# Performance work log

Hardware: AMD Instinct MI355X
Metric: run time of the kernel (lower is better)

Reference implementation:

```python
import jax, jax.numpy as jnp
import numpy as np

N = 50000
E = 800000
DIM_H = 128
EPS = 1e-5


def _glorot(key, shape):
    fan_in, fan_out = shape[0], shape[1]
    lim = np.sqrt(6.0 / (fan_in + fan_out))
    return jax.random.uniform(key, shape, jnp.float32, -lim, lim)


def setup_inputs() -> dict:
    key = jax.random.key(0)
    ks = jax.random.split(key, 12)
    h = jax.random.normal(ks[0], (N, DIM_H), jnp.float32)
    x = jax.random.normal(ks[1], (N, 3), jnp.float32)
    e = jax.random.randint(ks[2], (2, E), 0, N, jnp.int32)
    dx = jax.random.normal(ks[3], (E, 3), jnp.float32)
    d2 = jax.random.uniform(ks[4], (E, 1), jnp.float32)
    # message_layer.phi params: Linear(2*dim_h+1, dim_h), LayerNorm(dim_h), Linear(dim_h, dim_h)
    W1 = _glorot(ks[5], (2 * DIM_H + 1, DIM_H))
    b1 = jnp.zeros((DIM_H,), jnp.float32)
    g1 = jnp.ones((DIM_H,), jnp.float32)
    beta1 = jnp.zeros((DIM_H,), jnp.float32)
    W2 = _glorot(ks[6], (DIM_H, DIM_H))
    b2 = jnp.zeros((DIM_H,), jnp.float32)
    # outer phi params: Linear(dim_h, dim_h), Linear(dim_h, 1)
    W3 = _glorot(ks[7], (DIM_H, DIM_H))
    b3 = jnp.zeros((DIM_H,), jnp.float32)
    W4 = _glorot(ks[8], (DIM_H, 1))
    b4 = jnp.zeros((1,), jnp.float32)
    return {"h": h, "x": x, "e": e, "dx": dx, "d2": d2,
            "W1": W1, "b1": b1, "g1": g1, "beta1": beta1,
            "W2": W2, "b2": b2, "W3": W3, "b3": b3, "W4": W4, "b4": b4}


def _layernorm(z, g, b):
    mu = jnp.mean(z, axis=-1, keepdims=True)
    var = jnp.mean(jnp.square(z - mu), axis=-1, keepdims=True)
    return (z - mu) * jax.lax.rsqrt(var + EPS) * g + b


def reference(h, x, e, dx, d2, W1, b1, g1, beta1, W2, b2, W3, b3, W4, b4):
    ei, ej = e[0], e[1]
    hi = h[ei]                      # [E, dim_h]
    hj = h[ej]                      # [E, dim_h]
    msg = jnp.concatenate((hi, hj, d2), axis=-1)   # [E, 2*dim_h+1]
    msg = jax.nn.silu(msg @ W1 + b1)
    msg = _layernorm(msg, g1, beta1)
    msg = jax.nn.silu(msg @ W2 + b2)               # [E, dim_h]
    scale = jax.nn.silu(msg @ W3 + b3) @ W4 + b4   # [E, 1]
    vec = dx * scale                               # [E, 3]
    agg = jax.ops.segment_sum(vec, ei, num_segments=N)  # [N, 3]
    return x + agg
```

## Files before the change

kernel.cpp:

```cpp
#include <hip/hip_runtime.h>
#include <hip/hip_bf16.h>
#include <cstdint>

#define NN 50000
#define NE 800000
#define DH 128
#define TILES 50000
#define NCHUNK 4
#define CT (TILES / NCHUNK)

typedef __bf16 bf16;
typedef __bf16 bf16x8 __attribute__((ext_vector_type(8)));
typedef float  f32x4  __attribute__((ext_vector_type(4)));

__device__ __forceinline__ float fast_silu(float x) {
    float e = __expf(-x);
    return x * __builtin_amdgcn_rcpf(1.0f + e);
}

__global__ void prep_kernel(const float* __restrict__ W1, const float* __restrict__ W2,
                            const float* __restrict__ W3, const float* __restrict__ b1,
                            const float* __restrict__ g1, const float* __restrict__ bt1,
                            const float* __restrict__ b2, const float* __restrict__ b3,
                            const float* __restrict__ W4,
                            bf16* __restrict__ w1aT, bf16* __restrict__ w1bT,
                            bf16* __restrict__ w2T,  bf16* __restrict__ w3T,
                            float* __restrict__ smalls) {
    int i = blockIdx.x * 256 + threadIdx.x;
    int n = i >> 7, k = i & 127;
    w1aT[i] = (bf16)W1[k * DH + n];
    w1bT[i] = (bf16)W1[(k + DH) * DH + n];
    w2T[i]  = (bf16)W2[k * DH + n];
    w3T[i]  = (bf16)W3[k * DH + n];
    if (i < DH) {
        smalls[i]          = W1[256 * DH + i];
        smalls[DH + i]     = b1[i];
        smalls[2 * DH + i] = g1[i];
        smalls[3 * DH + i] = bt1[i];
        smalls[4 * DH + i] = b2[i];
        smalls[5 * DH + i] = b3[i];
        smalls[6 * DH + i] = W4[i];
    }
}

__global__ __launch_bounds__(256) void node_kernel(const float* __restrict__ h,
                                                   const bf16* __restrict__ w1aT,
                                                   const bf16* __restrict__ w1bT,
                                                   bf16* __restrict__ An,
                                                   bf16* __restrict__ Bn) {
    int lane = threadIdx.x & 63, wid = threadIdx.x >> 6;
    int r = lane & 15, g = lane >> 4;
    int wt = blockIdx.x * 4 + wid;
    if (wt >= (NN / 16)) return;
    int base = wt * 16;
    int node = base + r;

    bf16x8 ha[4];
#pragma unroll
    for (int s = 0; s < 4; s++) {
        const float* hp = h + (size_t)node * DH + s * 32 + g * 8;
        float4 p0 = *(const float4*)hp;
        float4 p1 = *(const float4*)(hp + 4);
        ha[s][0] = (bf16)p0.x; ha[s][1] = (bf16)p0.y;
        ha[s][2] = (bf16)p0.z; ha[s][3] = (bf16)p0.w;
        ha[s][4] = (bf16)p1.x; ha[s][5] = (bf16)p1.y;
        ha[s][6] = (bf16)p1.z; ha[s][7] = (bf16)p1.w;
    }
#pragma unroll
    for (int t = 0; t < 16; t++) {
        const bf16* wmat = (t < 8) ? w1aT : w1bT;
        int n = (t & 7) * 16 + r;
        f32x4 acc = {0.f, 0.f, 0.f, 0.f};
#pragma unroll
        for (int s = 0; s < 4; s++) {
            bf16x8 wb = *(const bf16x8*)(wmat + n * DH + s * 32 + g * 8);
            acc = __builtin_amdgcn_mfma_f32_16x16x32_bf16(ha[s], wb, acc, 0, 0, 0);
        }
        bf16* dst = (t < 8) ? An : Bn;
#pragma unroll
        for (int jj = 0; jj < 4; jj++)
            dst[(size_t)(base + g * 4 + jj) * DH + (t & 7) * 16 + r] = (bf16)acc[jj];
    }
}

__global__ void init_kernel(const float* __restrict__ x, float* __restrict__ out, int n) {
    int i = blockIdx.x * 256 + threadIdx.x;
    if (i < n) out[i] = x[i];
}

__global__ __launch_bounds__(256) void edgeA_kernel(
    const bf16* __restrict__ An, const bf16* __restrict__ Bn,
    const float* __restrict__ smalls, const int* __restrict__ e,
    const float* __restrict__ d2, bf16* __restrict__ Z, int tile0) {
    __shared__ float sSm[4 * 128];
    int tid = threadIdx.x;
    if (tid < 128) {
#pragma unroll
        for (int a = 0; a < 4; a++) sSm[a * 128 + tid] = smalls[a * 128 + tid];
    }
    __syncthreads();
    const float* s_w1c = sSm;
    const float* s_b1  = sSm + 128;
    const float* s_g1  = sSm + 256;
    const float* s_bt1 = sSm + 384;

    int lane = tid & 63, wid = tid >> 6;
    int r = lane & 15, g = lane >> 4;
    int wgid = blockIdx.x * 4 + wid;
    int nw = gridDim.x * 4;

    for (int lt = wgid; lt < CT; lt += nw) {
        int base = (tile0 + lt) * 16;
        int ei = e[base + r];
        int ej = e[NE + base + r];
        float d2v = d2[base + r];
        const bf16* Ar = An + (size_t)ei * DH;
        const bf16* Br = Bn + (size_t)ej * DH;

        float z[4][8];
#pragma unroll
        for (int s = 0; s < 4; s++) {
            bf16x8 av = *(const bf16x8*)(Ar + s * 32 + g * 8);
            bf16x8 bv = *(const bf16x8*)(Br + s * 32 + g * 8);
#pragma unroll
            for (int j = 0; j < 8; j++) {
                int f = s * 32 + g * 8 + j;
                float zz = (float)av[j] + (float)bv[j] + d2v * s_w1c[f] + s_b1[f];
                z[s][j] = fast_silu(zz);
            }
        }
        float sum = 0.f, sq = 0.f;
#pragma unroll
        for (int s = 0; s < 4; s++)
#pragma unroll
            for (int j = 0; j < 8; j++) { sum += z[s][j]; sq += z[s][j] * z[s][j]; }
        sum += __shfl_xor(sum, 16); sq += __shfl_xor(sq, 16);
        sum += __shfl_xor(sum, 32); sq += __shfl_xor(sq, 32);
        float mu = sum * 0.0078125f;
        float var = sq * 0.0078125f - mu * mu;
        float rs = __builtin_amdgcn_rsqf(var + 1e-5f);

        bf16* zp = Z + (size_t)lt * 2048 + g * 128 + r * 8;
#pragma unroll
        for (int s = 0; s < 4; s++) {
            bf16x8 af;
#pragma unroll
            for (int j = 0; j < 8; j++) {
                int f = s * 32 + g * 8 + j;
                af[j] = (bf16)((z[s][j] - mu) * rs * s_g1[f] + s_bt1[f]);
            }
            *(bf16x8*)(zp + s * 512) = af;
        }
    }
}

__global__ __launch_bounds__(512, 2) void edgeB_kernel(
    const bf16* __restrict__ Z, const bf16* __restrict__ w2T,
    const bf16* __restrict__ w3T, const float* __restrict__ smalls,
    const float* __restrict__ b4p, const int* __restrict__ e,
    const float* __restrict__ dxv, float* __restrict__ out, int tile0) {
    __shared__ __align__(16) bf16 sW2[128 * 136];
    __shared__ __align__(16) bf16 sY[8 * 16 * 136];
    __shared__ float sSm[3 * 128];

    int tid = threadIdx.x;
    for (int c = tid; c < 2048; c += 512) {
        int row = c >> 4, col = (c & 15) * 8;
        *(bf16x8*)&sW2[row * 136 + col] = *(const bf16x8*)&w2T[row * 128 + col];
    }
    if (tid < 128) {
#pragma unroll
        for (int a = 0; a < 3; a++) sSm[a * 128 + tid] = smalls[(4 + a) * 128 + tid];
    }
    __syncthreads();

    const float* s_b2 = sSm;
    const float* s_b3 = sSm + 128;
    const float* s_W4 = sSm + 256;
    float b4v = b4p[0];

    int lane = tid & 63, wid = tid >> 6;
    int r = lane & 15, g = lane >> 4;
    bf16* yw = &sY[wid * 16 * 136];
    const bf16* w3base = w3T + r * DH + g * 8;
    int wgid = blockIdx.x * 8 + wid;
    int nw = gridDim.x * 8;

    for (int lt = wgid; lt < CT; lt += nw) {
        int base = (tile0 + lt) * 16;
        int ei = e[base + r];

        const bf16* zp = Z + (size_t)lt * 2048 + g * 128 + r * 8;
        bf16x8 af[4];
#pragma unroll
        for (int s = 0; s < 4; s++) af[s] = *(const bf16x8*)(zp + s * 512);

#pragma unroll
        for (int t = 0; t < 8; t++) {
            f32x4 acc = {0.f, 0.f, 0.f, 0.f};
#pragma unroll
            for (int s = 0; s < 4; s++) {
                bf16x8 wb = *(const bf16x8*)&sW2[(t * 16 + r) * 136 + s * 32 + g * 8];
                acc = __builtin_amdgcn_mfma_f32_16x16x32_bf16(af[s], wb, acc, 0, 0, 0);
            }
            int n = t * 16 + r;
            float b2n = s_b2[n];
#pragma unroll
            for (int jj = 0; jj < 4; jj++)
                yw[(g * 4 + jj) * 136 + n] = (bf16)fast_silu(acc[jj] + b2n);
        }
        bf16x8 a2[4];
#pragma unroll
        for (int s = 0; s < 4; s++)
            a2[s] = *(const bf16x8*)&yw[r * 136 + s * 32 + g * 8];

        float part[4] = {0.f, 0.f, 0.f, 0.f};
#pragma unroll 4
        for (int t = 0; t < 8; t++) {
            f32x4 acc = {0.f, 0.f, 0.f, 0.f};
#pragma unroll
            for (int s = 0; s < 4; s++) {
                bf16x8 wb = *(const bf16x8*)(w3base + t * 16 * DH + s * 32);
                acc = __builtin_amdgcn_mfma_f32_16x16x32_bf16(a2[s], wb, acc, 0, 0, 0);
            }
            int n = t * 16 + r;
            float b3n = s_b3[n], w4n = s_W4[n];
#pragma unroll
            for (int jj = 0; jj < 4; jj++)
                part[jj] += fast_silu(acc[jj] + b3n) * w4n;
        }
#pragma unroll
        for (int jj = 0; jj < 4; jj++) {
            part[jj] += __shfl_xor(part[jj], 1);
            part[jj] += __shfl_xor(part[jj], 2);
            part[jj] += __shfl_xor(part[jj], 4);
            part[jj] += __shfl_xor(part[jj], 8);
        }
        {
            int m = lane >> 2, c3 = lane & 3;
            int jj = m & 3;
            float sc = (jj == 0) ? part[0] : (jj == 1) ? part[1]
                     : (jj == 2) ? part[2] : part[3];
            float scale = sc + b4v;
            int eim = __shfl(ei, m);
            if (c3 < 3)
                atomicAdd(&out[(size_t)eim * 3 + c3],
                          dxv[(size_t)(base + m) * 3 + c3] * scale);
        }
    }
}

extern "C" void kernel_launch(void* const* d_in, const int* in_sizes, int n_in,
                              void* d_out, int out_size, void* d_ws, size_t ws_size,
                              hipStream_t stream) {
    const float* h   = (const float*)d_in[0];
    const float* x   = (const float*)d_in[1];
    const int*   e   = (const int*)d_in[2];
    const float* dxv = (const float*)d_in[3];
    const float* d2  = (const float*)d_in[4];
    const float* W1  = (const float*)d_in[5];
    const float* b1  = (const float*)d_in[6];
    const float* g1  = (const float*)d_in[7];
    const float* bt1 = (const float*)d_in[8];
    const float* W2  = (const float*)d_in[9];
    const float* b2  = (const float*)d_in[10];
    const float* W3  = (const float*)d_in[11];
    const float* b3  = (const float*)d_in[12];
    const float* W4  = (const float*)d_in[13];
    const float* b4  = (const float*)d_in[14];

    char* ws = (char*)d_ws;
    bf16* An     = (bf16*)(ws);
    bf16* Bn     = (bf16*)(ws + 12800000);
    bf16* w1aT   = (bf16*)(ws + 25600000);
    bf16* w1bT   = (bf16*)(ws + 25632768);
    bf16* w2T    = (bf16*)(ws + 25665536);
    bf16* w3T    = (bf16*)(ws + 25698304);
    float* smalls = (float*)(ws + 25731072);
    bf16* Z      = (bf16*)(ws + 25734656);
    float* out   = (float*)d_out;

    prep_kernel<<<64, 256, 0, stream>>>(W1, W2, W3, b1, g1, bt1, b2, b3, W4,
                                        w1aT, w1bT, w2T, w3T, smalls);
    node_kernel<<<(NN / 16 + 3) / 4, 256, 0, stream>>>(h, w1aT, w1bT, An, Bn);
    init_kernel<<<(NN * 3 + 255) / 256, 256, 0, stream>>>(x, out, NN * 3);

    for (int c = 0; c < NCHUNK; ++c) {
        int tile0 = c * CT;
        edgeA_kernel<<<1024, 256, 0, stream>>>(An, Bn, smalls, e, d2, Z, tile0);
        edgeB_kernel<<<512, 512, 0, stream>>>(Z, w2T, w3T, smalls, b4,
                                              e, dxv, out, tile0);
    }
}
```

Before: 423.1 us.

## Restructure edgeB to 128-edge block tiles with register-resident weight fragments

edgeB now processes 128 edges per block: the Z tile is staged into shared memory, and each wave keeps its 16-column slice of W2 and W3 in registers instead of re-reading W2 from LDS and W3 from global memory for every 16-edge tile. The intermediate activations go to a shared buffer with an XOR-swizzled layout to avoid bank conflicts, and partial scale sums are reduced across waves in shared memory before the atomics. The chunk boundaries are rebalanced to 128-edge units. This adds block-wide barriers per tile and uses more LDS per block, which may lower occupancy.

Measured after the change: 484.6 us. 14.5% more time.

```diff
diff --git a/kernel.cpp b/kernel.cpp
--- a/kernel.cpp
+++ b/kernel.cpp
@@ -7,7 +7,6 @@
 #define DH 128
 #define TILES 50000
 #define NCHUNK 4
-#define CT (TILES / NCHUNK)
 
 typedef __bf16 bf16;
 typedef __bf16 bf16x8 __attribute__((ext_vector_type(8)));
@@ -91,7 +90,8 @@
 __global__ __launch_bounds__(256) void edgeA_kernel(
     const bf16* __restrict__ An, const bf16* __restrict__ Bn,
     const float* __restrict__ smalls, const int* __restrict__ e,
-    const float* __restrict__ d2, bf16* __restrict__ Z, int tile0) {
+    const float* __restrict__ d2, bf16* __restrict__ Z,
+    int tile0, int nt) {
     __shared__ float sSm[4 * 128];
     int tid = threadIdx.x;
     if (tid < 128) {
@@ -109,7 +109,7 @@
     int wgid = blockIdx.x * 4 + wid;
     int nw = gridDim.x * 4;
 
-    for (int lt = wgid; lt < CT; lt += nw) {
+    for (int lt = wgid; lt < nt; lt += nw) {
         int base = (tile0 + lt) * 16;
         int ei = e[base + r];
         int ej = e[NE + base + r];
@@ -158,94 +158,99 @@
     const bf16* __restrict__ Z, const bf16* __restrict__ w2T,
     const bf16* __restrict__ w3T, const float* __restrict__ smalls,
     const float* __restrict__ b4p, const int* __restrict__ e,
-    const float* __restrict__ dxv, float* __restrict__ out, int tile0) {
-    __shared__ __align__(16) bf16 sW2[128 * 136];
-    __shared__ __align__(16) bf16 sY[8 * 16 * 136];
-    __shared__ float sSm[3 * 128];
+    const float* __restrict__ dxv, float* __restrict__ out,
+    int t1280, int nt128) {
+    __shared__ __align__(16) bf16 sZ[128 * 128];
+    __shared__ __align__(16) bf16 sY[128 * 128];
+    __shared__ float sP[8 * 128];
+    __shared__ int sEi[128];
 
     int tid = threadIdx.x;
-    for (int c = tid; c < 2048; c += 512) {
-        int row = c >> 4, col = (c & 15) * 8;
-        *(bf16x8*)&sW2[row * 136 + col] = *(const bf16x8*)&w2T[row * 128 + col];
-    }
-    if (tid < 128) {
-#pragma unroll
-        for (int a = 0; a < 3; a++) sSm[a * 128 + tid] = smalls[(4 + a) * 128 + tid];
-    }
-    __syncthreads();
-
-    const float* s_b2 = sSm;
-    const float* s_b3 = sSm + 128;
-    const float* s_W4 = sSm + 256;
-    float b4v = b4p[0];
-
     int lane = tid & 63, wid = tid >> 6;
     int r = lane & 15, g = lane >> 4;
-    bf16* yw = &sY[wid * 16 * 136];
-    const bf16* w3base = w3T + r * DH + g * 8;
-    int wgid = blockIdx.x * 8 + wid;
-    int nw = gridDim.x * 8;
-
-    for (int lt = wgid; lt < CT; lt += nw) {
-        int base = (tile0 + lt) * 16;
-        int ei = e[base + r];
-
-        const bf16* zp = Z + (size_t)lt * 2048 + g * 128 + r * 8;
-        bf16x8 af[4];
-#pragma unroll
-        for (int s = 0; s < 4; s++) af[s] = *(const bf16x8*)(zp + s * 512);
-
-#pragma unroll
-        for (int t = 0; t < 8; t++) {
+
+    bf16x8 w2f[4], w3f[4];
+    {
+        const bf16* w2p = w2T + (16 * wid + r) * 128 + g * 8;
+        const bf16* w3p = w3T + (16 * wid + r) * 128 + g * 8;
+#pragma unroll
+        for (int s = 0; s < 4; s++) {
+            w2f[s] = *(const bf16x8*)(w2p + s * 32);
+            w3f[s] = *(const bf16x8*)(w3p + s * 32);
+        }
+    }
+    float b2v = smalls[512 + 16 * wid + r];
+    float b3v = smalls[640 + 16 * wid + r];
+    float w4v = smalls[768 + 16 * wid + r];
+    float b4v = b4p[0];
+
+    char* zb = (char*)sZ;
+    char* yb = (char*)sY;
+
+    for (int it = blockIdx.x; it < nt128; it += gridDim.x) {
+        size_t zbase = (size_t)it * 16384;
+        int ebase = (t1280 + it) * 128;
+
+        __syncthreads();
+        {
+            bf16x8 t0 = *(const bf16x8*)(Z + zbase + (size_t)(0 * 512 + tid) * 8);
+            bf16x8 t1 = *(const bf16x8*)(Z + zbase + (size_t)(1 * 512 + tid) * 8);
+            bf16x8 t2 = *(const bf16x8*)(Z + zbase + (size_t)(2 * 512 + tid) * 8);
+            bf16x8 t3 = *(const bf16x8*)(Z + zbase + (size_t)(3 * 512 + tid) * 8);
+            *(bf16x8*)&sZ[(0 * 512 + tid) * 8] = t0;
+            *(bf16x8*)&sZ[(1 * 512 + tid) * 8] = t1;
+            *(bf16x8*)&sZ[(2 * 512 + tid) * 8] = t2;
+            *(bf16x8*)&sZ[(3 * 512 + tid) * 8] = t3;
+            if (tid < 128) sEi[tid] = e[ebase + tid];
+        }
+        __syncthreads();
+
+#pragma unroll
+        for (int m = 0; m < 8; m++) {
             f32x4 acc = {0.f, 0.f, 0.f, 0.f};
 #pragma unroll
             for (int s = 0; s < 4; s++) {
-                bf16x8 wb = *(const bf16x8*)&sW2[(t * 16 + r) * 136 + s * 32 + g * 8];
-                acc = __builtin_amdgcn_mfma_f32_16x16x32_bf16(af[s], wb, acc, 0, 0, 0);
-            }
-            int n = t * 16 + r;
-            float b2n = s_b2[n];
-#pragma unroll
-            for (int jj = 0; jj < 4; jj++)
-                yw[(g * 4 + jj) * 136 + n] = (bf16)fast_silu(acc[jj] + b2n);
-        }
-        bf16x8 a2[4];
-#pragma unroll
-        for (int s = 0; s < 4; s++)
-            a2[s] = *(const bf16x8*)&yw[r * 136 + s * 32 + g * 8];
-
-        float part[4] = {0.f, 0.f, 0.f, 0.f};
-#pragma unroll 4
-        for (int t = 0; t < 8; t++) {
+                bf16x8 za = *(const bf16x8*)(zb + m * 4096 + s * 1024 + g * 256 + r * 16);
+                acc = __builtin_amdgcn_mfma_f32_16x16x32_bf16(za, w2f[s], acc, 0, 0, 0);
+            }
+            int nb = (16 * wid + r) * 2;
+#pragma unroll
+            for (int jj = 0; jj < 4; jj++) {
+                int edge = 16 * m + 4 * g + jj;
+                int addr = (edge * 256 + nb) ^ ((edge & 7) << 4);
+                *(bf16*)(yb + addr) = (bf16)fast_silu(acc[jj] + b2v);
+            }
+        }
+        __syncthreads();
+
+#pragma unroll
+        for (int m = 0; m < 8; m++) {
             f32x4 acc = {0.f, 0.f, 0.f, 0.f};
 #pragma unroll
             for (int s = 0; s < 4; s++) {
-                bf16x8 wb = *(const bf16x8*)(w3base + t * 16 * DH + s * 32);
-                acc = __builtin_amdgcn_mfma_f32_16x16x32_bf16(a2[s], wb, acc, 0, 0, 0);
-            }
-            int n = t * 16 + r;
-            float b3n = s_b3[n], w4n = s_W4[n];
-#pragma unroll
-            for (int jj = 0; jj < 4; jj++)
-                part[jj] += fast_silu(acc[jj] + b3n) * w4n;
-        }
-#pragma unroll
-        for (int jj = 0; jj < 4; jj++) {
-            part[jj] += __shfl_xor(part[jj], 1);
-            part[jj] += __shfl_xor(part[jj], 2);
-            part[jj] += __shfl_xor(part[jj], 4);
-            part[jj] += __shfl_xor(part[jj], 8);
-        }
-        {
-            int m = lane >> 2, c3 = lane & 3;
-            int jj = m & 3;
-            float sc = (jj == 0) ? part[0] : (jj == 1) ? part[1]
-                     : (jj == 2) ? part[2] : part[3];
-            float scale = sc + b4v;
-            int eim = __shfl(ei, m);
-            if (c3 < 3)
-                atomicAdd(&out[(size_t)eim * 3 + c3],
-                          dxv[(size_t)(base + m) * 3 + c3] * scale);
+                int addr = ((16 * m + r) * 256 + s * 64 + g * 16) ^ ((r & 7) << 4);
+                bf16x8 ya = *(const bf16x8*)(yb + addr);
+                acc = __builtin_amdgcn_mfma_f32_16x16x32_bf16(ya, w3f[s], acc, 0, 0, 0);
+            }
+#pragma unroll
+            for (int jj = 0; jj < 4; jj++) {
+                float v = fast_silu(acc[jj] + b3v) * w4v;
+                v += __shfl_xor(v, 1);
+                v += __shfl_xor(v, 2);
+                v += __shfl_xor(v, 4);
+                v += __shfl_xor(v, 8);
+                if (r == 0) sP[wid * 128 + 16 * m + 4 * g + jj] = v;
+            }
+        }
+        __syncthreads();
+
+        if (tid < 384) {
+            int eidx = tid & 127, c = tid >> 7;
+            float s = sP[eidx] + sP[128 + eidx] + sP[256 + eidx] + sP[384 + eidx]
+                    + sP[512 + eidx] + sP[640 + eidx] + sP[768 + eidx] + sP[896 + eidx];
+            float scale = s + b4v;
+            atomicAdd(&out[(size_t)sEi[eidx] * 3 + c],
+                      dxv[(size_t)(ebase + eidx) * 3 + c] * scale);
         }
     }
 }
@@ -285,10 +290,13 @@
     node_kernel<<<(NN / 16 + 3) / 4, 256, 0, stream>>>(h, w1aT, w1bT, An, Bn);
     init_kernel<<<(NN * 3 + 255) / 256, 256, 0, stream>>>(x, out, NN * 3);
 
+    int starts[NCHUNK + 1] = {0, 1563, 3126, 4688, 6250};
     for (int c = 0; c < NCHUNK; ++c) {
-        int tile0 = c * CT;
-        edgeA_kernel<<<1024, 256, 0, stream>>>(An, Bn, smalls, e, d2, Z, tile0);
+        int t1280 = starts[c];
+        int nt128 = starts[c + 1] - starts[c];
+        edgeA_kernel<<<1024, 256, 0, stream>>>(An, Bn, smalls, e, d2, Z,
+                                               t1280 * 8, nt128 * 8);
         edgeB_kernel<<<512, 512, 0, stream>>>(Z, w2T, w3T, smalls, b4,
-                                              e, dxv, out, tile0);
-    }
-}
+                                              e, dxv, out, t1280, nt128);
+    }
+}
```
